# Kernel tuning notes

Measured on AMD Instinct MI355X. Metric: run time of the kernel, lower is better.

Reference implementation:

```python
import jax, jax.numpy as jnp
import numpy as np
from math import sqrt

N_HEADS = 4
IN_FEATURES = 64
KQ = 64
HEAD_V = IN_FEATURES // N_HEADS  # 16


def setup_inputs() -> dict:
    key = jax.random.key(0)
    ks = jax.random.split(key, 7)
    s = 0.05
    x = jax.random.normal(ks[0], (8192, IN_FEATURES), dtype=jnp.float32)
    # Per-head Linear weights stacked on a leading head axis.
    # torch Linear: y = x @ W.T + b; we store W already transposed: [H, F, E]
    Wq = jax.random.normal(ks[1], (N_HEADS, IN_FEATURES, KQ), dtype=jnp.float32) * s
    bq = jax.random.normal(ks[2], (N_HEADS, KQ), dtype=jnp.float32) * s
    Wk = jax.random.normal(ks[3], (N_HEADS, IN_FEATURES, KQ), dtype=jnp.float32) * s
    bk = jax.random.normal(ks[4], (N_HEADS, KQ), dtype=jnp.float32) * s
    Wv = jax.random.normal(ks[5], (N_HEADS, IN_FEATURES, HEAD_V), dtype=jnp.float32) * s
    bv = jax.random.normal(ks[6], (N_HEADS, HEAD_V), dtype=jnp.float32) * s
    return {"x": x, "Wq": Wq, "bq": bq, "Wk": Wk, "bk": bk, "Wv": Wv, "bv": bv}


def reference(x, Wq, bq, Wk, bk, Wv, bv):
    N, F = x.shape
    scale = 1.0 / sqrt(F)  # original divides by sqrt(in_features), NOT sqrt(kq)
    # Batched-head projections: [H, N, E]
    Q = jnp.einsum('nf,hfe->hne', x, Wq) + bq[:, None, :]
    K = jnp.einsum('nf,hfe->hne', x, Wk) + bk[:, None, :]
    V = jnp.einsum('nf,hfd->hnd', x, Wv) + bv[:, None, :]
    logits = jnp.einsum('hne,hme->hnm', Q, K) * scale  # [H, N, N]
    attn = jax.nn.softmax(logits, axis=-1)
    out_heads = jnp.einsum('hnm,hmd->hnd', attn, V)    # [H, N, HEAD_V]
    # Head i writes columns [i*HEAD_V:(i+1)*HEAD_V] of the output.
    out = jnp.transpose(out_heads, (1, 0, 2)).reshape(N, F)
    return out
```

## Files before the change

### kernel.cpp

```cpp
#include <hip/hip_runtime.h>

typedef __attribute__((ext_vector_type(4))) float f32x4;
typedef __attribute__((ext_vector_type(8))) short bf16x8;
typedef __attribute__((ext_vector_type(4))) short bf16x4;
typedef long fp8x8;

#define NH 4

static __device__ __forceinline__ unsigned short f2bf(float f){
  unsigned u = __float_as_uint(f);
  u += 0x7FFFu + ((u >> 16) & 1u);
  return (unsigned short)(u >> 16);
}

static __device__ __forceinline__ unsigned pack2bf(float a, float b){
  return __builtin_amdgcn_perm(__float_as_uint(b) + 0x8000u,
                               __float_as_uint(a) + 0x8000u, 0x07060302u);
}

static __device__ __forceinline__ unsigned pack2bf_t(float a, float b){
  return __builtin_amdgcn_perm(__float_as_uint(b), __float_as_uint(a), 0x07060302u);
}

static __device__ __forceinline__ int pack_fp8x4(float a, float b, float c, float d){
  int w = __builtin_amdgcn_cvt_pk_fp8_f32(a, b, 0, false);
  w     = __builtin_amdgcn_cvt_pk_fp8_f32(c, d, w, true);
  return w;
}

__global__ __launch_bounds__(256) void wprep_kernel(
    const float* __restrict__ Wq, const float* __restrict__ bq,
    const float* __restrict__ Wk, const float* __restrict__ bk,
    const float* __restrict__ Wv,
    unsigned short* __restrict__ WF, float* __restrict__ bias_s, int n)
{
  __shared__ unsigned short wqT[64*72];
  __shared__ unsigned short wkT[64*72];
  __shared__ unsigned short wvT[16*72];

  const int t = threadIdx.x;
  const int h = blockIdx.x;
  const float S1 = 0.4246609001f;
  const int f = t >> 2, eg = t & 3;

  {
    const float4* g = (const float4*)(Wq + h*4096 + f*64 + eg*16);
    #pragma unroll
    for (int p = 0; p < 4; ++p){
      float4 d = g[p];
      int e0 = eg*16 + p*4;
      wqT[(e0+0)*72 + f] = f2bf(d.x * S1);
      wqT[(e0+1)*72 + f] = f2bf(d.y * S1);
      wqT[(e0+2)*72 + f] = f2bf(d.z * S1);
      wqT[(e0+3)*72 + f] = f2bf(d.w * S1);
    }
  }
  {
    const float4* g = (const float4*)(Wk + h*4096 + f*64 + eg*16);
    #pragma unroll
    for (int p = 0; p < 4; ++p){
      float4 d = g[p];
      int e0 = eg*16 + p*4;
      wkT[(e0+0)*72 + f] = f2bf(d.x * S1);
      wkT[(e0+1)*72 + f] = f2bf(d.y * S1);
      wkT[(e0+2)*72 + f] = f2bf(d.z * S1);
      wkT[(e0+3)*72 + f] = f2bf(d.w * S1);
    }
  }
  {
    float4 d = *(const float4*)(Wv + h*1024 + f*16 + eg*4);
    int d0 = eg*4;
    wvT[(d0+0)*72 + f] = f2bf(d.x);
    wvT[(d0+1)*72 + f] = f2bf(d.y);
    wvT[(d0+2)*72 + f] = f2bf(d.z);
    wvT[(d0+3)*72 + f] = f2bf(d.w);
  }
  if (t < 64)       bias_s[h*128 + t] = bq[h*64 + t] * S1;
  else if (t < 128) bias_s[h*128 + t] = bk[h*64 + (t-64)] * S1;
  __syncthreads();

  const int lane = t & 63, w = t >> 6;
  const int quad = lane >> 4, l16 = lane & 15;
  for (int s = w; s < 18; s += 4){
    const unsigned short* src;
    if (s < 8){      int et = s>>1,     ks = s&1;     src = wqT + (et*16+l16)*72 + ks*32 + quad*8; }
    else if (s < 16){int ft = (s-8)>>1, ks = (s-8)&1; src = wkT + (ft*16+l16)*72 + ks*32 + quad*8; }
    else {           int ks = s-16;                   src = wvT + l16*72 + ks*32 + quad*8; }
    uint4 v = *(const uint4*)src;
    *(uint4*)(WF + ((size_t)(h*18 + s)*64 + lane)*8) = v;
  }
}

__global__ __launch_bounds__(256) void proj_kernel(
    const float* __restrict__ x, const float* __restrict__ bv,
    const unsigned short* __restrict__ WF, const float* __restrict__ bias_s,
    unsigned char* __restrict__ Qfr, unsigned char* __restrict__ Kt,
    unsigned short* __restrict__ Vt, int n)
{
  __shared__ unsigned short xf[8*64*8];
  __shared__ float bql[64], bkl[64], bvl[16];

  const int t  = threadIdx.x;
  const int h  = blockIdx.y;
  const int r0 = blockIdx.x * 64;

  {
    const int r = t >> 2, cg4 = t & 3;
    const float4* g = (const float4*)(x + (size_t)(r0 + r)*64 + cg4*16);
    float4 a = g[0], b = g[1], c = g[2], d = g[3];
    unsigned u0 = pack2bf(a.x,a.y), u1 = pack2bf(a.z,a.w);
    unsigned u2 = pack2bf(b.x,b.y), u3 = pack2bf(b.z,b.w);
    unsigned u4 = pack2bf(c.x,c.y), u5 = pack2bf(c.z,c.w);
    unsigned u6 = pack2bf(d.x,d.y), u7 = pack2bf(d.z,d.w);
    const int it = r >> 4, l16r = r & 15, ks = cg4 >> 1, q0 = (cg4 & 1)*2;
    uint4* dst0 = (uint4*)(xf + ((it*2+ks)*64 + q0*16     + l16r)*8);
    uint4* dst1 = (uint4*)(xf + ((it*2+ks)*64 + (q0+1)*16 + l16r)*8);
    *dst0 = make_uint4(u0,u1,u2,u3);
    *dst1 = make_uint4(u4,u5,u6,u7);
  }
  if (t < 64)        bql[t]     = bias_s[h*128 + t];
  else if (t < 128)  bkl[t-64]  = bias_s[h*128 + t];
  else if (t < 144)  bvl[t-128] = bv[h*16 + (t-128)];
  __syncthreads();

  const int lane = t & 63, w = t >> 6;
  const int quad = lane >> 4, l16 = lane & 15;

  bf16x8 xa[8];
  #pragma unroll
  for (int i = 0; i < 8; ++i)
    xa[i] = *(const bf16x8*)(xf + (i*64 + lane)*8);

  const unsigned short* WFh = WF + (size_t)h*18*64*8;
  bf16x8 wq0 = *(const bf16x8*)(WFh + ((size_t)(     w*2 + 0)*64 + lane)*8);
  bf16x8 wq1 = *(const bf16x8*)(WFh + ((size_t)(     w*2 + 1)*64 + lane)*8);
  bf16x8 wk0 = *(const bf16x8*)(WFh + ((size_t)(8  + w*2 + 0)*64 + lane)*8);
  bf16x8 wk1 = *(const bf16x8*)(WFh + ((size_t)(8  + w*2 + 1)*64 + lane)*8);
  bf16x8 wv0 = *(const bf16x8*)(WFh + ((size_t)16*64 + lane)*8);
  bf16x8 wv1 = *(const bf16x8*)(WFh + ((size_t)17*64 + lane)*8);

  const f32x4 z = {0.f,0.f,0.f,0.f};
  f32x4 accQ[4] = {z,z,z,z};
  f32x4 accK[4] = {z,z,z,z};
  f32x4 accV = z;

  #pragma unroll
  for (int it = 0; it < 4; ++it){
    accQ[it] = __builtin_amdgcn_mfma_f32_16x16x32_bf16(wq0, xa[it*2+0], accQ[it], 0,0,0);
    accQ[it] = __builtin_amdgcn_mfma_f32_16x16x32_bf16(wq1, xa[it*2+1], accQ[it], 0,0,0);
  }
  #pragma unroll
  for (int tt = 0; tt < 4; ++tt){
    accK[tt] = __builtin_amdgcn_mfma_f32_16x16x32_bf16(wk0, xa[tt*2+0], accK[tt], 0,0,0);
    accK[tt] = __builtin_amdgcn_mfma_f32_16x16x32_bf16(wk1, xa[tt*2+1], accK[tt], 0,0,0);
  }
  accV = __builtin_amdgcn_mfma_f32_16x16x32_bf16(xa[w*2+0], wv0, accV, 0,0,0);
  accV = __builtin_amdgcn_mfma_f32_16x16x32_bf16(xa[w*2+1], wv1, accV, 0,0,0);

  {
    const int e0 = w*16 + quad*4;
    const float b0 = bql[e0], b1 = bql[e0+1], b2 = bql[e0+2], b3 = bql[e0+3];
    const int qk = (e0 & 31) >> 3, hf = e0 >> 5, boff = (quad & 1) * 4;
    #pragma unroll
    for (int it = 0; it < 4; ++it){
      unsigned o = pack_fp8x4(accQ[it][0]+b0, accQ[it][1]+b1,
                              accQ[it][2]+b2, accQ[it][3]+b3);
      const int T = (r0 >> 4) + it;
      *(unsigned*)(Qfr + (size_t)h*((size_t)n<<6) + (size_t)T*1024
                       + (qk*16 + l16)*16 + hf*8 + boff) = o;
    }
  }
  {
    const int f0 = w*16 + quad*4;
    const float bk0 = bkl[f0], bk1 = bkl[f0+1], bk2 = bkl[f0+2], bk3 = bkl[f0+3];
    const int qk = (f0 & 31) >> 3, hf = f0 >> 5, boff = (quad & 1) * 4;
    #pragma unroll
    for (int tt = 0; tt < 4; ++tt){
      unsigned o = pack_fp8x4(accK[tt][0]+bk0, accK[tt][1]+bk1,
                              accK[tt][2]+bk2, accK[tt][3]+bk3);
      const int T = (r0 >> 4) + tt;
      *(unsigned*)(Kt + (size_t)h*((size_t)n<<6) + (size_t)T*1024
                      + (qk*16 + l16)*16 + hf*8 + boff) = o;
    }
  }
  {
    float bvv = bvl[l16];
    unsigned v01 = pack2bf(accV[0]+bvv, accV[1]+bvv);
    unsigned v23 = pack2bf(accV[2]+bvv, accV[3]+bvv);
    const int T = (r0 >> 4) + w;
    *(uint2*)(Vt + (size_t)h*((size_t)n<<4) + ((size_t)T*64 + lane)*4) = make_uint2(v01, v23);
  }
}

__global__ __launch_bounds__(512, 8) void attn_kernel(
    const unsigned char* __restrict__ Qfr, const unsigned char* __restrict__ Kt,
    const unsigned short* __restrict__ Vt, float* __restrict__ out, int n)
{
  __shared__ float part[7][64][17];

  const int tid  = threadIdx.x;
  const int lane = tid & 63;
  const int jq   = tid >> 6;
  const int bid  = blockIdx.x;
  const int h    = bid & 3;
  const int iblk = bid >> 2;
  const int l16  = lane & 15, quad = lane >> 4;
  const int i0   = iblk*32;
  const int ntq  = (n >> 3) >> 4;
  const int tile0 = jq * ntq;

  const unsigned char* qfh = Qfr + (size_t)h*((size_t)n<<6);
  longlong2 q0 = *(const longlong2*)(qfh + (size_t)((i0>>4)    )*1024 + lane*16);
  longlong2 q1 = *(const longlong2*)(qfh + (size_t)((i0>>4) + 1)*1024 + lane*16);
  const fp8x8 qf00 = (fp8x8)q0.x;
  const fp8x8 qf01 = (fp8x8)q0.y;
  const fp8x8 qf10 = (fp8x8)q1.x;
  const fp8x8 qf11 = (fp8x8)q1.y;

  const longlong2* ktl = (const longlong2*)(Kt + (size_t)h*((size_t)n<<6)) + (size_t)tile0*64 + lane;
  const uint2*     vtu = (const uint2*)(Vt + (size_t)h*((size_t)n<<4)) + (size_t)tile0*64 + lane;

  f32x4 o0  = {0.f,0.f,0.f,0.f};
  f32x4 o1  = {0.f,0.f,0.f,0.f};
  f32x4 la0 = {0.f,0.f,0.f,0.f};
  f32x4 la1 = {0.f,0.f,0.f,0.f};
  const f32x4 z = {0.f,0.f,0.f,0.f};
  const bf16x4 vones = {(short)0x3F80, (short)0x3F80, (short)0x3F80, (short)0x3F80};

  longlong2 ka = ktl[0];
  uint2     va = vtu[0];
  longlong2 kb = ktl[64];
  uint2     vb = vtu[64];

#define ATTN_TILE(KK, VV)                                                     \
  {                                                                           \
    fp8x8 k0 = (fp8x8)KK.x;                                                   \
    fp8x8 k1 = (fp8x8)KK.y;                                                   \
    bf16x4 vf; { union { uint2 u; bf16x4 v; } c; c.u = VV; vf = c.v; }        \
    f32x4 s0 = __builtin_amdgcn_mfma_f32_16x16x32_fp8_fp8(k0, qf00, z, 0,0,0);\
    s0 = __builtin_amdgcn_mfma_f32_16x16x32_fp8_fp8(k1, qf01, s0, 0,0,0);     \
    f32x4 s1 = __builtin_amdgcn_mfma_f32_16x16x32_fp8_fp8(k0, qf10, z, 0,0,0);\
    s1 = __builtin_amdgcn_mfma_f32_16x16x32_fp8_fp8(k1, qf11, s1, 0,0,0);     \
    float p00 = __builtin_amdgcn_exp2f(s0[0]);                                \
    float p01 = __builtin_amdgcn_exp2f(s0[1]);                                \
    float p02 = __builtin_amdgcn_exp2f(s0[2]);                                \
    float p03 = __builtin_amdgcn_exp2f(s0[3]);                                \
    float p10 = __builtin_amdgcn_exp2f(s1[0]);                                \
    float p11 = __builtin_amdgcn_exp2f(s1[1]);                                \
    float p12 = __builtin_amdgcn_exp2f(s1[2]);                                \
    float p13 = __builtin_amdgcn_exp2f(s1[3]);                                \
    union { uint2 u; bf16x4 v; } pc0, pc1;                                    \
    pc0.u = make_uint2(pack2bf_t(p00,p01), pack2bf_t(p02,p03));               \
    pc1.u = make_uint2(pack2bf_t(p10,p11), pack2bf_t(p12,p13));               \
    o0  = __builtin_amdgcn_mfma_f32_16x16x16bf16_1k(pc0.v, vf,    o0,  0,0,0);\
    o1  = __builtin_amdgcn_mfma_f32_16x16x16bf16_1k(pc1.v, vf,    o1,  0,0,0);\
    la0 = __builtin_amdgcn_mfma_f32_16x16x16bf16_1k(pc0.v, vones, la0, 0,0,0);\
    la1 = __builtin_amdgcn_mfma_f32_16x16x16bf16_1k(pc1.v, vones, la1, 0,0,0);\
  }

  for (int tt = 0; tt < ntq - 2; tt += 2){
    longlong2 kc = ktl[128];
    uint2     vc = vtu[128];
    longlong2 kd = ktl[192];
    uint2     vd = vtu[192];
    ATTN_TILE(ka, va)
    ATTN_TILE(kb, vb)
    ka = kc; va = vc;
    kb = kd; vb = vd;
    ktl += 128; vtu += 128;
  }
  ATTN_TILE(ka, va)
  ATTN_TILE(kb, vb)
#undef ATTN_TILE

  if (jq > 0){
    float* p = &part[jq-1][lane][0];
    p[ 0]=o0[0];  p[ 1]=o0[1];  p[ 2]=o0[2];  p[ 3]=o0[3];
    p[ 4]=o1[0];  p[ 5]=o1[1];  p[ 6]=o1[2];  p[ 7]=o1[3];
    p[ 8]=la0[0]; p[ 9]=la0[1]; p[10]=la0[2]; p[11]=la0[3];
    p[12]=la1[0]; p[13]=la1[1]; p[14]=la1[2]; p[15]=la1[3];
  }
  __syncthreads();

  if (jq == 0){
    #pragma unroll
    for (int q = 0; q < 7; ++q){
      const float* r = &part[q][lane][0];
      o0[0] +=r[0];  o0[1] +=r[1];  o0[2] +=r[2];  o0[3] +=r[3];
      o1[0] +=r[4];  o1[1] +=r[5];  o1[2] +=r[6];  o1[3] +=r[7];
      la0[0]+=r[8];  la0[1]+=r[9];  la0[2]+=r[10]; la0[3]+=r[11];
      la1[0]+=r[12]; la1[1]+=r[13]; la1[2]+=r[14]; la1[3]+=r[15];
    }
    #pragma unroll
    for (int reg = 0; reg < 4; ++reg){
      int i = quad*4 + reg;
      out[(size_t)(i0 + i)*64      + h*16 + l16] = o0[reg] / la0[reg];
      out[(size_t)(i0 + 16 + i)*64 + h*16 + l16] = o1[reg] / la1[reg];
    }
  }
}

extern "C" void kernel_launch(void* const* d_in, const int* in_sizes, int n_in,
                              void* d_out, int out_size, void* d_ws, size_t ws_size,
                              hipStream_t stream) {
  const float* x  = (const float*)d_in[0];
  const float* Wq = (const float*)d_in[1];
  const float* bq = (const float*)d_in[2];
  const float* Wk = (const float*)d_in[3];
  const float* bk = (const float*)d_in[4];
  const float* Wv = (const float*)d_in[5];
  const float* bv = (const float*)d_in[6];
  float* out = (float*)d_out;

  const int n = in_sizes[0] / 64;

  unsigned char* Qfr  = (unsigned char*)d_ws;
  unsigned char* Kt   = Qfr + (size_t)NH*n*64;
  unsigned short* Vt  = (unsigned short*)(Kt + (size_t)NH*n*64);
  unsigned short* WF  = Vt + (size_t)NH*n*16;
  float* bias_s       = (float*)(WF + (size_t)NH*18*64*8);

  wprep_kernel<<<NH, 256, 0, stream>>>(Wq, bq, Wk, bk, Wv, WF, bias_s, n);
  proj_kernel<<<dim3(n/64, NH), 256, 0, stream>>>(x, bv, WF, bias_s, Qfr, Kt, Vt, n);
  attn_kernel<<<dim3((n/32)*NH), 512, 0, stream>>>(Qfr, Kt, Vt, out, n);
}
```

Measured before the change: 121.8 us.

## Use 16x16x32 bf16 MFMA for PV and compute row sums on VALU

```diff
diff --git a/kernel.cpp b/kernel.cpp
--- a/kernel.cpp
+++ b/kernel.cpp
@@ -188,7 +188,9 @@
     unsigned v01 = pack2bf(accV[0]+bvv, accV[1]+bvv);
     unsigned v23 = pack2bf(accV[2]+bvv, accV[3]+bvv);
     const int T = (r0 >> 4) + w;
-    *(uint2*)(Vt + (size_t)h*((size_t)n<<4) + ((size_t)T*64 + lane)*4) = make_uint2(v01, v23);
+    unsigned short* dst = Vt + (size_t)h*((size_t)n<<4)
+                        + (size_t)(T>>1)*512 + lane*8 + (T&1)*4;
+    *(uint2*)dst = make_uint2(v01, v23);
   }
 }
 
@@ -196,7 +198,7 @@
     const unsigned char* __restrict__ Qfr, const unsigned char* __restrict__ Kt,
     const unsigned short* __restrict__ Vt, float* __restrict__ out, int n)
 {
-  __shared__ float part[7][64][17];
+  __shared__ float part[7][64][11];
 
   const int tid  = threadIdx.x;
   const int lane = tid & 63;
@@ -206,8 +208,7 @@
   const int iblk = bid >> 2;
   const int l16  = lane & 15, quad = lane >> 4;
   const int i0   = iblk*32;
-  const int ntq  = (n >> 3) >> 4;
-  const int tile0 = jq * ntq;
+  const int ngq  = (n >> 3) >> 5;
 
   const unsigned char* qfh = Qfr + (size_t)h*((size_t)n<<6);
   longlong2 q0 = *(const longlong2*)(qfh + (size_t)((i0>>4)    )*1024 + lane*16);
@@ -217,68 +218,84 @@
   const fp8x8 qf10 = (fp8x8)q1.x;
   const fp8x8 qf11 = (fp8x8)q1.y;
 
-  const longlong2* ktl = (const longlong2*)(Kt + (size_t)h*((size_t)n<<6)) + (size_t)tile0*64 + lane;
-  const uint2*     vtu = (const uint2*)(Vt + (size_t)h*((size_t)n<<4)) + (size_t)tile0*64 + lane;
-
-  f32x4 o0  = {0.f,0.f,0.f,0.f};
-  f32x4 o1  = {0.f,0.f,0.f,0.f};
-  f32x4 la0 = {0.f,0.f,0.f,0.f};
-  f32x4 la1 = {0.f,0.f,0.f,0.f};
+  const longlong2* ktl = (const longlong2*)(Kt + (size_t)h*((size_t)n<<6))
+                       + (size_t)(jq*ngq)*128 + lane;
+  const uint4*     vtu = (const uint4*)(Vt + (size_t)h*((size_t)n<<4))
+                       + (size_t)(jq*ngq)*64 + lane;
+
+  f32x4 o0 = {0.f,0.f,0.f,0.f};
+  f32x4 o1 = {0.f,0.f,0.f,0.f};
+  float ls0 = 0.f, ls1 = 0.f;
   const f32x4 z = {0.f,0.f,0.f,0.f};
-  const bf16x4 vones = {(short)0x3F80, (short)0x3F80, (short)0x3F80, (short)0x3F80};
-
-  longlong2 ka = ktl[0];
-  uint2     va = vtu[0];
-  longlong2 kb = ktl[64];
-  uint2     vb = vtu[64];
-
-#define ATTN_TILE(KK, VV)                                                     \
+
+#define PROC_GROUP(KT0, KT1, VG)                                              \
   {                                                                           \
-    fp8x8 k0 = (fp8x8)KK.x;                                                   \
-    fp8x8 k1 = (fp8x8)KK.y;                                                   \
-    bf16x4 vf; { union { uint2 u; bf16x4 v; } c; c.u = VV; vf = c.v; }        \
-    f32x4 s0 = __builtin_amdgcn_mfma_f32_16x16x32_fp8_fp8(k0, qf00, z, 0,0,0);\
-    s0 = __builtin_amdgcn_mfma_f32_16x16x32_fp8_fp8(k1, qf01, s0, 0,0,0);     \
-    f32x4 s1 = __builtin_amdgcn_mfma_f32_16x16x32_fp8_fp8(k0, qf10, z, 0,0,0);\
-    s1 = __builtin_amdgcn_mfma_f32_16x16x32_fp8_fp8(k1, qf11, s1, 0,0,0);     \
-    float p00 = __builtin_amdgcn_exp2f(s0[0]);                                \
-    float p01 = __builtin_amdgcn_exp2f(s0[1]);                                \
-    float p02 = __builtin_amdgcn_exp2f(s0[2]);                                \
-    float p03 = __builtin_amdgcn_exp2f(s0[3]);                                \
-    float p10 = __builtin_amdgcn_exp2f(s1[0]);                                \
-    float p11 = __builtin_amdgcn_exp2f(s1[1]);                                \
-    float p12 = __builtin_amdgcn_exp2f(s1[2]);                                \
-    float p13 = __builtin_amdgcn_exp2f(s1[3]);                                \
-    union { uint2 u; bf16x4 v; } pc0, pc1;                                    \
-    pc0.u = make_uint2(pack2bf_t(p00,p01), pack2bf_t(p02,p03));               \
-    pc1.u = make_uint2(pack2bf_t(p10,p11), pack2bf_t(p12,p13));               \
-    o0  = __builtin_amdgcn_mfma_f32_16x16x16bf16_1k(pc0.v, vf,    o0,  0,0,0);\
-    o1  = __builtin_amdgcn_mfma_f32_16x16x16bf16_1k(pc1.v, vf,    o1,  0,0,0);\
-    la0 = __builtin_amdgcn_mfma_f32_16x16x16bf16_1k(pc0.v, vones, la0, 0,0,0);\
-    la1 = __builtin_amdgcn_mfma_f32_16x16x16bf16_1k(pc1.v, vones, la1, 0,0,0);\
-  }
-
-  for (int tt = 0; tt < ntq - 2; tt += 2){
-    longlong2 kc = ktl[128];
-    uint2     vc = vtu[128];
-    longlong2 kd = ktl[192];
-    uint2     vd = vtu[192];
-    ATTN_TILE(ka, va)
-    ATTN_TILE(kb, vb)
-    ka = kc; va = vc;
-    kb = kd; vb = vd;
-    ktl += 128; vtu += 128;
-  }
-  ATTN_TILE(ka, va)
-  ATTN_TILE(kb, vb)
-#undef ATTN_TILE
+    fp8x8 ak0 = (fp8x8)KT0.x, ak1 = (fp8x8)KT0.y;                             \
+    fp8x8 bk0 = (fp8x8)KT1.x, bk1 = (fp8x8)KT1.y;                             \
+    f32x4 sa0 = __builtin_amdgcn_mfma_f32_16x16x32_fp8_fp8(ak0, qf00, z,0,0,0);\
+    sa0 = __builtin_amdgcn_mfma_f32_16x16x32_fp8_fp8(ak1, qf01, sa0, 0,0,0);  \
+    f32x4 sa1 = __builtin_amdgcn_mfma_f32_16x16x32_fp8_fp8(ak0, qf10, z,0,0,0);\
+    sa1 = __builtin_amdgcn_mfma_f32_16x16x32_fp8_fp8(ak1, qf11, sa1, 0,0,0);  \
+    f32x4 sb0 = __builtin_amdgcn_mfma_f32_16x16x32_fp8_fp8(bk0, qf00, z,0,0,0);\
+    sb0 = __builtin_amdgcn_mfma_f32_16x16x32_fp8_fp8(bk1, qf01, sb0, 0,0,0);  \
+    f32x4 sb1 = __builtin_amdgcn_mfma_f32_16x16x32_fp8_fp8(bk0, qf10, z,0,0,0);\
+    sb1 = __builtin_amdgcn_mfma_f32_16x16x32_fp8_fp8(bk1, qf11, sb1, 0,0,0);  \
+    float pa00 = __builtin_amdgcn_exp2f(sa0[0]);                              \
+    float pa01 = __builtin_amdgcn_exp2f(sa0[1]);                              \
+    float pa02 = __builtin_amdgcn_exp2f(sa0[2]);                              \
+    float pa03 = __builtin_amdgcn_exp2f(sa0[3]);                              \
+    float pa10 = __builtin_amdgcn_exp2f(sa1[0]);                              \
+    float pa11 = __builtin_amdgcn_exp2f(sa1[1]);                              \
+    float pa12 = __builtin_amdgcn_exp2f(sa1[2]);                              \
+    float pa13 = __builtin_amdgcn_exp2f(sa1[3]);                              \
+    float pb00 = __builtin_amdgcn_exp2f(sb0[0]);                              \
+    float pb01 = __builtin_amdgcn_exp2f(sb0[1]);                              \
+    float pb02 = __builtin_amdgcn_exp2f(sb0[2]);                              \
+    float pb03 = __builtin_amdgcn_exp2f(sb0[3]);                              \
+    float pb10 = __builtin_amdgcn_exp2f(sb1[0]);                              \
+    float pb11 = __builtin_amdgcn_exp2f(sb1[1]);                              \
+    float pb12 = __builtin_amdgcn_exp2f(sb1[2]);                              \
+    float pb13 = __builtin_amdgcn_exp2f(sb1[3]);                              \
+    ls0 += ((pa00 + pa01) + (pa02 + pa03)) + ((pb00 + pb01) + (pb02 + pb03)); \
+    ls1 += ((pa10 + pa11) + (pa12 + pa13)) + ((pb10 + pb11) + (pb12 + pb13)); \
+    union { unsigned u[4]; bf16x8 v; } af0, af1;                              \
+    af0.u[0] = pack2bf_t(pa00,pa01); af0.u[1] = pack2bf_t(pa02,pa03);         \
+    af0.u[2] = pack2bf_t(pb00,pb01); af0.u[3] = pack2bf_t(pb02,pb03);         \
+    af1.u[0] = pack2bf_t(pa10,pa11); af1.u[1] = pack2bf_t(pa12,pa13);         \
+    af1.u[2] = pack2bf_t(pb10,pb11); af1.u[3] = pack2bf_t(pb12,pb13);         \
+    bf16x8 vgf; { union { uint4 u; bf16x8 v; } c; c.u = VG; vgf = c.v; }      \
+    o0 = __builtin_amdgcn_mfma_f32_16x16x32_bf16(af0.v, vgf, o0, 0,0,0);      \
+    o1 = __builtin_amdgcn_mfma_f32_16x16x32_bf16(af1.v, vgf, o1, 0,0,0);      \
+  }
+
+  longlong2 kA0 = ktl[0],   kA1 = ktl[64];
+  uint4     vA  = vtu[0];
+  longlong2 kB0 = ktl[128], kB1 = ktl[192];
+  uint4     vB  = vtu[64];
+
+  for (int g = 0; g < ngq - 2; g += 2){
+    longlong2 kC0 = ktl[256], kC1 = ktl[320];
+    uint4     vC  = vtu[128];
+    longlong2 kD0 = ktl[384], kD1 = ktl[448];
+    uint4     vD  = vtu[192];
+    PROC_GROUP(kA0, kA1, vA)
+    PROC_GROUP(kB0, kB1, vB)
+    kA0 = kC0; kA1 = kC1; vA = vC;
+    kB0 = kD0; kB1 = kD1; vB = vD;
+    ktl += 256; vtu += 128;
+  }
+  PROC_GROUP(kA0, kA1, vA)
+  PROC_GROUP(kB0, kB1, vB)
+#undef PROC_GROUP
+
+  ls0 += __shfl_xor(ls0, 16); ls0 += __shfl_xor(ls0, 32);
+  ls1 += __shfl_xor(ls1, 16); ls1 += __shfl_xor(ls1, 32);
 
   if (jq > 0){
     float* p = &part[jq-1][lane][0];
-    p[ 0]=o0[0];  p[ 1]=o0[1];  p[ 2]=o0[2];  p[ 3]=o0[3];
-    p[ 4]=o1[0];  p[ 5]=o1[1];  p[ 6]=o1[2];  p[ 7]=o1[3];
-    p[ 8]=la0[0]; p[ 9]=la0[1]; p[10]=la0[2]; p[11]=la0[3];
-    p[12]=la1[0]; p[13]=la1[1]; p[14]=la1[2]; p[15]=la1[3];
+    p[0]=o0[0]; p[1]=o0[1]; p[2]=o0[2]; p[3]=o0[3];
+    p[4]=o1[0]; p[5]=o1[1]; p[6]=o1[2]; p[7]=o1[3];
+    p[8]=ls0;   p[9]=ls1;
   }
   __syncthreads();
 
@@ -286,16 +303,19 @@
     #pragma unroll
     for (int q = 0; q < 7; ++q){
       const float* r = &part[q][lane][0];
-      o0[0] +=r[0];  o0[1] +=r[1];  o0[2] +=r[2];  o0[3] +=r[3];
-      o1[0] +=r[4];  o1[1] +=r[5];  o1[2] +=r[6];  o1[3] +=r[7];
-      la0[0]+=r[8];  la0[1]+=r[9];  la0[2]+=r[10]; la0[3]+=r[11];
-      la1[0]+=r[12]; la1[1]+=r[13]; la1[2]+=r[14]; la1[3]+=r[15];
-    }
+      o0[0]+=r[0]; o0[1]+=r[1]; o0[2]+=r[2]; o0[3]+=r[3];
+      o1[0]+=r[4]; o1[1]+=r[5]; o1[2]+=r[6]; o1[3]+=r[7];
+      ls0 += r[8]; ls1 += r[9];
+    }
+    float inv0 = 1.0f / ls0;
+    float inv1 = 1.0f / ls1;
     #pragma unroll
     for (int reg = 0; reg < 4; ++reg){
       int i = quad*4 + reg;
-      out[(size_t)(i0 + i)*64      + h*16 + l16] = o0[reg] / la0[reg];
-      out[(size_t)(i0 + 16 + i)*64 + h*16 + l16] = o1[reg] / la1[reg];
+      float a0 = __shfl(inv0, i);
+      float a1 = __shfl(inv1, i);
+      out[(size_t)(i0 + i)*64      + h*16 + l16] = o0[reg] * a0;
+      out[(size_t)(i0 + 16 + i)*64 + h*16 + l16] = o1[reg] * a1;
     }
   }
 }
```

Result: slower. 151.8 us (+24.6%).
